# Performance work log

Measured on AMD Instinct MI355X. Metric: run time of the kernel, lower is better.

The kernel has to match this reference:

```python
import jax, jax.numpy as jnp
import numpy as np
import math

B, S, D, H, N = 4, 2048, 1024, 8, 128  # batch, seq_len, d_model, n_heads, num_osc
ITERS = 10
DT = 0.1
PI = math.pi


def setup_inputs() -> dict:
    key = jax.random.key(0)
    ks = jax.random.split(key, 5)
    return {
        "x": jax.random.normal(ks[0], (B, S, D), jnp.float32),
        "mask": jnp.ones((B, S), jnp.int32),
        "W_phase": jax.random.normal(ks[1], (D, H * N), jnp.float32) / math.sqrt(D),
        "b_phase": jnp.zeros((H * N,), jnp.float32),
        "natural_freq": jax.random.normal(ks[2], (H, N), jnp.float32) * 0.1,
        "coupling": jnp.ones((H, 1, 1), jnp.float32),  # coupling_strength = 1.0
        "W_out": jax.random.normal(ks[3], (H * N, D), jnp.float32) / math.sqrt(H * N),
        "b_out": jnp.zeros((D,), jnp.float32),
    }


def reference(x, mask, W_phase, b_phase, natural_freq, coupling, W_out, b_out):
    # phases: [B, H, S, N]
    ph = (x @ W_phase + b_phase).reshape(B, S, H, N).transpose(0, 2, 1, 3)
    ph = jnp.tanh(ph) * PI
    m = mask.astype(ph.dtype)[:, None, :, None]  # [B,1,S,1] mask over j
    K = coupling.reshape(1, H, 1, 1)
    w = natural_freq.reshape(1, H, 1, N)

    def step(ph, _):
        s = jnp.sin(ph)
        c = jnp.cos(ph)
        # mean_j m_j * sin(theta_i - theta_j) = sin(th_i)*mean(m*cos) - cos(th_i)*mean(m*sin)
        ms = (m * s).mean(axis=2, keepdims=True)  # [B,H,1,N]
        mc = (m * c).mean(axis=2, keepdims=True)
        dtheta = w + K * (s * mc - c * ms)
        ph2 = jnp.mod(ph + DT * dtheta + PI, 2 * PI) - PI
        return ph2, None

    ph, _ = jax.lax.scan(step, ph, None, length=ITERS)
    # from_phase; dropout is identity in eval mode
    y = ph.transpose(0, 2, 1, 3).reshape(B, S, H * N) @ W_out + b_out
    return y
```

## Files before the change

kernel.cpp:

```cpp
#include <hip/hip_runtime.h>
#include <math.h>

#define S_ 2048
#define D_ 1024
#define HN_ 1024
#define B_ 4
#define M_ 8192
#define K1_ 3072
#define K3_ 1024
#define ITERS_ 10
#define DT_ 0.1f
#define PI_ 3.14159265358979323846f
#define TWOPI_ 6.28318530717958647692f
#define INV2PI_ 0.15915494309189533577f
#define SCALE_ 4096.0f
#define INVSC2_ (1.0f / 16777216.0f)

typedef __attribute__((ext_vector_type(8))) _Float16 f16x8;
typedef __attribute__((ext_vector_type(4))) float f32x4;

__device__ ushort g_xs [(size_t)M_ * K1_];
__device__ ushort g_WpT[(size_t)HN_ * K1_];
__device__ float  g_ph [(size_t)B_ * HN_ * S_];
__device__ ushort g_phh[(size_t)B_ * HN_ * S_];
__device__ ushort g_phT[(size_t)M_ * HN_];
__device__ ushort g_WoT[(size_t)D_ * HN_];

__device__ __forceinline__ ushort f2h(float f) {
    union { _Float16 h; ushort u; } v; v.h = (_Float16)f; return v.u;
}
__device__ __forceinline__ void split2s(float x, ushort& A, ushort& Bc) {
    const float xs = x * SCALE_;
    union { _Float16 h; ushort u; } va, vb;
    va.h = (_Float16)xs;
    const float r = xs - (float)va.h;
    vb.h = (_Float16)r;
    A = va.u; Bc = vb.u;
}
__device__ __forceinline__ void gload16(const void* g, void* l) {
    __builtin_amdgcn_global_load_lds(
        (const __attribute__((address_space(1))) void*)g,
        (__attribute__((address_space(3))) void*)l, 16, 0, 0);
}
__device__ __forceinline__ int pack2(ushort a, ushort b) {
    return (int)(unsigned)a | ((int)(unsigned)b << 16);
}

__global__ __launch_bounds__(256) void split_x(const float* __restrict__ X) {
    const int idx = blockIdx.x * 256 + threadIdx.x;
    const float4 v = ((const float4*)X)[idx];
    const int m  = idx >> 8;
    const int k4 = (idx & 255) * 4;
    ushort a[4], b[4];
    split2s(v.x, a[0], b[0]);
    split2s(v.y, a[1], b[1]);
    split2s(v.z, a[2], b[2]);
    split2s(v.w, a[3], b[3]);
    ushort* row = g_xs + (size_t)m * K1_ + k4;
    int2 oa; oa.x = pack2(a[0], a[1]); oa.y = pack2(a[2], a[3]);
    int2 ob; ob.x = pack2(b[0], b[1]); ob.y = pack2(b[2], b[3]);
    *(int2*)(row)        = oa;
    *(int2*)(row + 1024) = oa;
    *(int2*)(row + 2048) = ob;
}

__global__ __launch_bounds__(256) void splitT_Wp(const float* __restrict__ Wp) {
    __shared__ float t[64][68];
    const int k0 = blockIdx.x * 64;
    const int n0 = blockIdx.y * 64;
    const int r = threadIdx.x >> 2;
    const int c = (threadIdx.x & 3) * 16;
    const float* src = Wp + (size_t)(k0 + r) * HN_ + n0 + c;
    #pragma unroll
    for (int q = 0; q < 4; ++q)
        *(float4*)&t[r][c + 4 * q] = ((const float4*)src)[q];
    __syncthreads();
    ushort ha[16], hb[16];
    #pragma unroll
    for (int j = 0; j < 16; ++j)
        split2s(t[c + j][r], ha[j], hb[j]);
    int4 a0, a1, b0, b1;
    a0.x = pack2(ha[0], ha[1]);   a0.y = pack2(ha[2], ha[3]);
    a0.z = pack2(ha[4], ha[5]);   a0.w = pack2(ha[6], ha[7]);
    a1.x = pack2(ha[8], ha[9]);   a1.y = pack2(ha[10], ha[11]);
    a1.z = pack2(ha[12], ha[13]); a1.w = pack2(ha[14], ha[15]);
    b0.x = pack2(hb[0], hb[1]);   b0.y = pack2(hb[2], hb[3]);
    b0.z = pack2(hb[4], hb[5]);   b0.w = pack2(hb[6], hb[7]);
    b1.x = pack2(hb[8], hb[9]);   b1.y = pack2(hb[10], hb[11]);
    b1.z = pack2(hb[12], hb[13]); b1.w = pack2(hb[14], hb[15]);
    ushort* dst = g_WpT + (size_t)(n0 + r) * K1_ + k0 + c;
    *(int4*)(dst)            = a0; *(int4*)(dst + 8)        = a1;
    *(int4*)(dst + 1024)     = b0; *(int4*)(dst + 1032)     = b1;
    *(int4*)(dst + 2048)     = a0; *(int4*)(dst + 2056)     = a1;
}

__global__ __launch_bounds__(256) void castT_Wo(const float* __restrict__ Wo) {
    __shared__ float t[64][68];
    const int k0 = blockIdx.x * 64;
    const int n0 = blockIdx.y * 64;
    const int r = threadIdx.x >> 2;
    const int c = (threadIdx.x & 3) * 16;
    const float* src = Wo + (size_t)(k0 + r) * D_ + n0 + c;
    #pragma unroll
    for (int q = 0; q < 4; ++q)
        *(float4*)&t[r][c + 4 * q] = ((const float4*)src)[q];
    __syncthreads();
    ushort h[16];
    #pragma unroll
    for (int j = 0; j < 16; ++j) h[j] = f2h(t[c + j][r]);
    ushort* dst = g_WoT + (size_t)(n0 + r) * HN_ + k0 + c;
    int4 o0, o1;
    o0.x = pack2(h[0], h[1]);   o0.y = pack2(h[2], h[3]);
    o0.z = pack2(h[4], h[5]);   o0.w = pack2(h[6], h[7]);
    o1.x = pack2(h[8], h[9]);   o1.y = pack2(h[10], h[11]);
    o1.z = pack2(h[12], h[13]); o1.w = pack2(h[14], h[15]);
    *(int4*)dst = o0;
    *(int4*)(dst + 8) = o1;
}

template<int KDIM>
__device__ __forceinline__ void gemm_mainloop(const ushort* __restrict__ A,
                                              const ushort* __restrict__ Bm,
                                              ushort* lds,
                                              int m0, int n0, int wid, int l,
                                              int wm, int wn,
                                              f32x4 (&acc)[4][2]) {
    constexpr int NT = KDIM / 64;
    const int r8   = l >> 3;
    const int swzo = ((l & 7) * 16) ^ (r8 << 4);
    const char* gA = (const char*)(A + (size_t)m0 * KDIM);
    const char* gB = (const char*)(Bm + (size_t)n0 * KDIM);

    const int l15 = l & 15;
    const int xk  = (l15 & 7) << 4;
    const int sl0 = (((l >> 4) * 16)) ^ xk;
    const int sl1 = (64 + ((l >> 4) * 16)) ^ xk;
    const char* pA = (const char*)lds + (wm * 64 + l15) * 128;
    const char* pB = (const char*)lds + 16384 + (wn * 32 + l15) * 128;

    #define STAGE(T, BUF) do {                                                    \
        const size_t gb_ = (size_t)(T) * 128 + swzo;                              \
        char* lb_ = (char*)lds + (BUF) * 32768 + wid * 2048;                      \
        gload16(gA + (size_t)(wid * 16 + r8)     * (KDIM * 2) + gb_, lb_);        \
        gload16(gA + (size_t)(wid * 16 + 8 + r8) * (KDIM * 2) + gb_, lb_ + 1024); \
        gload16(gB + (size_t)(wid * 16 + r8)     * (KDIM * 2) + gb_, lb_ + 16384);\
        gload16(gB + (size_t)(wid * 16 + 8 + r8) * (KDIM * 2) + gb_, lb_ + 16384 + 1024); \
    } while (0)

    STAGE(0, 0);

    #pragma unroll 2
    for (int t = 0; t < NT; ++t) {
        __builtin_amdgcn_sched_barrier(0);
        __builtin_amdgcn_s_barrier();
        __builtin_amdgcn_sched_barrier(0);
        if (t + 1 < NT) {
            STAGE(t + 1, (t + 1) & 1);
            asm volatile("s_waitcnt vmcnt(4)" ::: "memory");
        } else {
            asm volatile("s_waitcnt vmcnt(0)" ::: "memory");
        }
        __builtin_amdgcn_sched_barrier(0);
        __builtin_amdgcn_s_barrier();
        __builtin_amdgcn_sched_barrier(0);

        const int bo = (t & 1) << 15;
        f16x8 Aa[4][2], Bb[2][2];
        #pragma unroll
        for (int i = 0; i < 4; ++i) {
            Aa[i][0] = *(const f16x8*)(pA + bo + i * 2048 + sl0);
            Aa[i][1] = *(const f16x8*)(pA + bo + i * 2048 + sl1);
        }
        #pragma unroll
        for (int j = 0; j < 2; ++j) {
            Bb[j][0] = *(const f16x8*)(pB + bo + j * 2048 + sl0);
            Bb[j][1] = *(const f16x8*)(pB + bo + j * 2048 + sl1);
        }
        __builtin_amdgcn_s_setprio(1);
        #pragma unroll
        for (int ks = 0; ks < 2; ++ks)
            #pragma unroll
            for (int i = 0; i < 4; ++i)
                #pragma unroll
                for (int j = 0; j < 2; ++j)
                    acc[i][j] = __builtin_amdgcn_mfma_f32_16x16x32_f16(
                        Aa[i][ks], Bb[j][ks], acc[i][j], 0, 0, 0);
        __builtin_amdgcn_s_setprio(0);
    }
    #undef STAGE
}

__device__ __forceinline__ void tile_map(int bid, int& m0, int& n0) {
    const int xcd = bid & 7;
    const int idx = bid >> 3;
    m0 = (xcd * 8 + (idx >> 3)) * 128;
    n0 = (idx & 7) * 128;
}

__global__ __launch_bounds__(512, 4) void gemm1(const float* __restrict__ bias) {
    __shared__ ushort lds[2 * 16384];
    const int tid = threadIdx.x;
    const int wid = tid >> 6, l = tid & 63;
    int m0, n0;
    tile_map(blockIdx.x, m0, n0);
    const int wm = wid >> 2, wn = wid & 3;

    f32x4 acc[4][2];
    #pragma unroll
    for (int i = 0; i < 4; ++i)
        #pragma unroll
        for (int j = 0; j < 2; ++j) acc[i][j] = (f32x4){0.f, 0.f, 0.f, 0.f};

    gemm_mainloop<K1_>(g_xs, g_WpT, lds, m0, n0, wid, l, wm, wn, acc);

    const int r4 = (l >> 4) * 4;
    const int cn = l & 15;
    #pragma unroll
    for (int i = 0; i < 4; ++i) {
        const int mg = m0 + wm * 64 + i * 16 + r4;
        const int bidx = mg >> 11;
        const int sg = mg & 2047;
        #pragma unroll
        for (int jj = 0; jj < 2; ++jj) {
            const int ng = n0 + wn * 32 + jj * 16 + cn;
            const float bb = bias[ng];
            float4 o;
            o.x = PI_ * tanhf(fmaf(acc[i][jj][0], INVSC2_, bb));
            o.y = PI_ * tanhf(fmaf(acc[i][jj][1], INVSC2_, bb));
            o.z = PI_ * tanhf(fmaf(acc[i][jj][2], INVSC2_, bb));
            o.w = PI_ * tanhf(fmaf(acc[i][jj][3], INVSC2_, bb));
            *(float4*)(g_ph + ((size_t)bidx * HN_ + ng) * S_ + sg) = o;
        }
    }
}

__global__ __launch_bounds__(512, 4) void gemm3(const float* __restrict__ bias,
                                                float* __restrict__ Y) {
    __shared__ ushort lds[2 * 16384];
    const int tid = threadIdx.x;
    const int wid = tid >> 6, l = tid & 63;
    int m0, n0;
    tile_map(blockIdx.x, m0, n0);
    const int wm = wid >> 2, wn = wid & 3;

    f32x4 acc[4][2];
    #pragma unroll
    for (int i = 0; i < 4; ++i)
        #pragma unroll
        for (int j = 0; j < 2; ++j) acc[i][j] = (f32x4){0.f, 0.f, 0.f, 0.f};

    gemm_mainloop<K3_>(g_phT, g_WoT, lds, m0, n0, wid, l, wm, wn, acc);

    const int r4 = (l >> 4) * 4;
    const int cn = l & 15;
    #pragma unroll
    for (int i = 0; i < 4; ++i) {
        const int mg = m0 + wm * 64 + i * 16 + r4;
        #pragma unroll
        for (int jj = 0; jj < 2; ++jj) {
            const int ng = n0 + wn * 32 + jj * 16 + cn;
            const float bb = bias[ng];
            #pragma unroll
            for (int r = 0; r < 4; ++r)
                Y[(size_t)(mg + r) * D_ + ng] = acc[i][jj][r] + bb;
        }
    }
}

__global__ __launch_bounds__(256) void kuramoto(const int* __restrict__ mask,
                                                const float* __restrict__ natf,
                                                const float* __restrict__ coup) {
    const int wave = blockIdx.x * 4 + (threadIdx.x >> 6);
    const int lane = threadIdx.x & 63;
    const int b = wave >> 10;
    const int hn = wave & 1023;
    const int h = hn >> 7;

    const float wf = natf[hn];
    const float K = coup[h];

    const float* base = g_ph + ((size_t)b * HN_ + hn) * S_;

    float ph[32];
    #pragma unroll
    for (int i = 0; i < 8; ++i) {
        float4 v = *(const float4*)(base + i * 256 + lane * 4);
        ph[4 * i + 0] = v.x; ph[4 * i + 1] = v.y;
        ph[4 * i + 2] = v.z; ph[4 * i + 3] = v.w;
    }

    const int* mb = mask + b * S_;
    unsigned mbits = 0;
    #pragma unroll
    for (int i = 0; i < 8; ++i) {
        int4 mv = *(const int4*)(mb + i * 256 + lane * 4);
        mbits |= (mv.x != 0 ? 1u : 0u) << (4 * i + 0);
        mbits |= (mv.y != 0 ? 1u : 0u) << (4 * i + 1);
        mbits |= (mv.z != 0 ? 1u : 0u) << (4 * i + 2);
        mbits |= (mv.w != 0 ? 1u : 0u) << (4 * i + 3);
    }

    for (int it = 0; it < ITERS_; ++it) {
        float s[32], c[32];
        float ls = 0.f, lc = 0.f;
        #pragma unroll
        for (int i = 0; i < 32; ++i) {
            s[i] = __sinf(ph[i]);
            c[i] = __cosf(ph[i]);
            const float mf = (float)((mbits >> i) & 1u);
            ls = fmaf(mf, s[i], ls);
            lc = fmaf(mf, c[i], lc);
        }
        #pragma unroll
        for (int off = 32; off; off >>= 1) {
            ls += __shfl_xor(ls, off);
            lc += __shfl_xor(lc, off);
        }
        const float ms = ls * (1.f / 2048.f);
        const float mc = lc * (1.f / 2048.f);
        #pragma unroll
        for (int i = 0; i < 32; ++i) {
            const float dth = fmaf(K, fmaf(s[i], mc, -c[i] * ms), wf);
            float t = fmaf(DT_, dth, ph[i]) + PI_;
            t -= TWOPI_ * floorf(t * INV2PI_);
            ph[i] = t - PI_;
        }
    }

    ushort* ob = g_phh + ((size_t)b * HN_ + hn) * S_;
    #pragma unroll
    for (int i = 0; i < 8; ++i) {
        ushort4 o;
        o.x = f2h(ph[4 * i + 0]); o.y = f2h(ph[4 * i + 1]);
        o.z = f2h(ph[4 * i + 2]); o.w = f2h(ph[4 * i + 3]);
        *(ushort4*)(ob + i * 256 + lane * 4) = o;
    }
}

__global__ __launch_bounds__(256) void transpose_ph() {
    __shared__ ushort t[64][72];
    const int b = blockIdx.z;
    const int h0 = blockIdx.y * 64;
    const int s0 = blockIdx.x * 64;
    const int r = threadIdx.x >> 2;
    const int c = (threadIdx.x & 3) * 16;
    const ushort* src = g_phh + ((size_t)b * HN_ + h0 + r) * S_ + s0 + c;
    *(int4*)&t[r][c] = *(const int4*)src;
    *(int4*)&t[r][c + 8] = *(const int4*)(src + 8);
    __syncthreads();
    ushort o[16];
    #pragma unroll
    for (int j = 0; j < 16; ++j) o[j] = t[c + j][r];
    ushort* dst = g_phT + ((size_t)(b * S_ + s0 + r)) * HN_ + h0 + c;
    int4 o0, o1;
    o0.x = pack2(o[0], o[1]);   o0.y = pack2(o[2], o[3]);
    o0.z = pack2(o[4], o[5]);   o0.w = pack2(o[6], o[7]);
    o1.x = pack2(o[8], o[9]);   o1.y = pack2(o[10], o[11]);
    o1.z = pack2(o[12], o[13]); o1.w = pack2(o[14], o[15]);
    *(int4*)dst = o0;
    *(int4*)(dst + 8) = o1;
}

extern "C" void kernel_launch(void* const* d_in, const int* in_sizes, int n_in,
                              void* d_out, int out_size, void* d_ws, size_t ws_size,
                              hipStream_t stream) {
    const float* x    = (const float*)d_in[0];
    const int*   mask = (const int*)d_in[1];
    const float* Wp   = (const float*)d_in[2];
    const float* bp   = (const float*)d_in[3];
    const float* natf = (const float*)d_in[4];
    const float* coup = (const float*)d_in[5];
    const float* Wo   = (const float*)d_in[6];
    const float* bo   = (const float*)d_in[7];
    float* y = (float*)d_out;

    split_x  <<<dim3(8192),         256, 0, stream>>>(x);
    splitT_Wp<<<dim3(16, 16),       256, 0, stream>>>(Wp);
    castT_Wo <<<dim3(16, 16),       256, 0, stream>>>(Wo);
    gemm1    <<<dim3(512),          512, 0, stream>>>(bp);
    kuramoto <<<dim3(1024),         256, 0, stream>>>(mask, natf, coup);
    transpose_ph<<<dim3(32, 16, 4), 256, 0, stream>>>();
    gemm3    <<<dim3(512),          512, 0, stream>>>(bo, y);
}
```

Before: 166.2 us.

## Pre-fragment weights into MFMA register layout and load B directly from global

Weights are repacked into a fragment-major layout so each lane can load its MFMA B operand straight from global memory into registers, with no LDS staging. The split-fp16 A operand shrinks from three copies to two (hi and lo), and the loop visits the hi part twice, once against the weight hi and once against the weight lo. LDS use per block is halved and the main loop is unrolled by two with explicit double buffering. B loads now go through the vector memory path, which may add latency and repeat global traffic across blocks that share the same weights.

```diff
diff --git a/kernel.cpp b/kernel.cpp
--- a/kernel.cpp
+++ b/kernel.cpp
@@ -6,8 +6,6 @@
 #define HN_ 1024
 #define B_ 4
 #define M_ 8192
-#define K1_ 3072
-#define K3_ 1024
 #define ITERS_ 10
 #define DT_ 0.1f
 #define PI_ 3.14159265358979323846f
@@ -19,12 +17,12 @@
 typedef __attribute__((ext_vector_type(8))) _Float16 f16x8;
 typedef __attribute__((ext_vector_type(4))) float f32x4;
 
-__device__ ushort g_xs [(size_t)M_ * K1_];
-__device__ ushort g_WpT[(size_t)HN_ * K1_];
-__device__ float  g_ph [(size_t)B_ * HN_ * S_];
-__device__ ushort g_phh[(size_t)B_ * HN_ * S_];
-__device__ ushort g_phT[(size_t)M_ * HN_];
-__device__ ushort g_WoT[(size_t)D_ * HN_];
+__device__ __align__(16) ushort g_xs [(size_t)M_ * 2048];
+__device__ __align__(16) ushort g_WpB[(size_t)64 * 64 * 512];
+__device__ __align__(16) ushort g_WoB[(size_t)64 * 32 * 512];
+__device__ __align__(16) float  g_ph [(size_t)B_ * HN_ * S_];
+__device__ __align__(16) ushort g_phh[(size_t)B_ * HN_ * S_];
+__device__ __align__(16) ushort g_phT[(size_t)M_ * HN_];
 
 __device__ __forceinline__ ushort f2h(float f) {
     union { _Float16 h; ushort u; } v; v.h = (_Float16)f; return v.u;
@@ -56,138 +54,158 @@
     split2s(v.y, a[1], b[1]);
     split2s(v.z, a[2], b[2]);
     split2s(v.w, a[3], b[3]);
-    ushort* row = g_xs + (size_t)m * K1_ + k4;
+    ushort* row = g_xs + (size_t)m * 2048 + k4;
     int2 oa; oa.x = pack2(a[0], a[1]); oa.y = pack2(a[2], a[3]);
     int2 ob; ob.x = pack2(b[0], b[1]); ob.y = pack2(b[2], b[3]);
     *(int2*)(row)        = oa;
-    *(int2*)(row + 1024) = oa;
-    *(int2*)(row + 2048) = ob;
-}
-
-__global__ __launch_bounds__(256) void splitT_Wp(const float* __restrict__ Wp) {
-    __shared__ float t[64][68];
-    const int k0 = blockIdx.x * 64;
-    const int n0 = blockIdx.y * 64;
-    const int r = threadIdx.x >> 2;
-    const int c = (threadIdx.x & 3) * 16;
-    const float* src = Wp + (size_t)(k0 + r) * HN_ + n0 + c;
-    #pragma unroll
-    for (int q = 0; q < 4; ++q)
-        *(float4*)&t[r][c + 4 * q] = ((const float4*)src)[q];
+    *(int2*)(row + 1024) = ob;
+}
+
+__global__ __launch_bounds__(128) void prep_WpB(const float* __restrict__ Wp) {
+    __shared__ float t[64][17];
+    const int kc = blockIdx.x, n16 = blockIdx.y;
+    const int k0 = kc * 64, nb = n16 * 16;
+    {
+        const int r = threadIdx.x >> 1, hf = (threadIdx.x & 1) * 8;
+        const float* src = Wp + (size_t)(k0 + r) * HN_ + nb + hf;
+        *(float4*)&t[r][hf]     = *(const float4*)src;
+        *(float4*)&t[r][hf + 4] = *(const float4*)(src + 4);
+    }
     __syncthreads();
-    ushort ha[16], hb[16];
-    #pragma unroll
-    for (int j = 0; j < 16; ++j)
-        split2s(t[c + j][r], ha[j], hb[j]);
-    int4 a0, a1, b0, b1;
-    a0.x = pack2(ha[0], ha[1]);   a0.y = pack2(ha[2], ha[3]);
-    a0.z = pack2(ha[4], ha[5]);   a0.w = pack2(ha[6], ha[7]);
-    a1.x = pack2(ha[8], ha[9]);   a1.y = pack2(ha[10], ha[11]);
-    a1.z = pack2(ha[12], ha[13]); a1.w = pack2(ha[14], ha[15]);
-    b0.x = pack2(hb[0], hb[1]);   b0.y = pack2(hb[2], hb[3]);
-    b0.z = pack2(hb[4], hb[5]);   b0.w = pack2(hb[6], hb[7]);
-    b1.x = pack2(hb[8], hb[9]);   b1.y = pack2(hb[10], hb[11]);
-    b1.z = pack2(hb[12], hb[13]); b1.w = pack2(hb[14], hb[15]);
-    ushort* dst = g_WpT + (size_t)(n0 + r) * K1_ + k0 + c;
-    *(int4*)(dst)            = a0; *(int4*)(dst + 8)        = a1;
-    *(int4*)(dst + 1024)     = b0; *(int4*)(dst + 1032)     = b1;
-    *(int4*)(dst + 2048)     = a0; *(int4*)(dst + 2056)     = a1;
-}
-
-__global__ __launch_bounds__(256) void castT_Wo(const float* __restrict__ Wo) {
-    __shared__ float t[64][68];
-    const int k0 = blockIdx.x * 64;
-    const int n0 = blockIdx.y * 64;
-    const int r = threadIdx.x >> 2;
-    const int c = (threadIdx.x & 3) * 16;
-    const float* src = Wo + (size_t)(k0 + r) * D_ + n0 + c;
-    #pragma unroll
-    for (int q = 0; q < 4; ++q)
-        *(float4*)&t[r][c + 4 * q] = ((const float4*)src)[q];
+    const int h = threadIdx.x >> 6, l = threadIdx.x & 63;
+    const int n = l & 15, ks8 = (l >> 4) * 8;
+    ushort ua[8], ub[8];
+    #pragma unroll
+    for (int j = 0; j < 8; ++j)
+        split2s(t[h * 32 + ks8 + j][n], ua[j], ub[j]);
+    const int kt32a = kc * 2 + h;
+    ushort* da = g_WpB + ((size_t)(n16 * 64 + kt32a) * 64 + l) * 8;
+    ushort* db = g_WpB + ((size_t)(n16 * 64 + 32 + kt32a) * 64 + l) * 8;
+    int4 oa, ob;
+    oa.x = pack2(ua[0], ua[1]); oa.y = pack2(ua[2], ua[3]);
+    oa.z = pack2(ua[4], ua[5]); oa.w = pack2(ua[6], ua[7]);
+    ob.x = pack2(ub[0], ub[1]); ob.y = pack2(ub[2], ub[3]);
+    ob.z = pack2(ub[4], ub[5]); ob.w = pack2(ub[6], ub[7]);
+    *(int4*)da = oa;
+    *(int4*)db = ob;
+}
+
+__global__ __launch_bounds__(128) void prep_WoB(const float* __restrict__ Wo) {
+    __shared__ float t[64][17];
+    const int kc = blockIdx.x, n16 = blockIdx.y;
+    const int k0 = kc * 64, nb = n16 * 16;
+    {
+        const int r = threadIdx.x >> 1, hf = (threadIdx.x & 1) * 8;
+        const float* src = Wo + (size_t)(k0 + r) * D_ + nb + hf;
+        *(float4*)&t[r][hf]     = *(const float4*)src;
+        *(float4*)&t[r][hf + 4] = *(const float4*)(src + 4);
+    }
     __syncthreads();
-    ushort h[16];
-    #pragma unroll
-    for (int j = 0; j < 16; ++j) h[j] = f2h(t[c + j][r]);
-    ushort* dst = g_WoT + (size_t)(n0 + r) * HN_ + k0 + c;
-    int4 o0, o1;
-    o0.x = pack2(h[0], h[1]);   o0.y = pack2(h[2], h[3]);
-    o0.z = pack2(h[4], h[5]);   o0.w = pack2(h[6], h[7]);
-    o1.x = pack2(h[8], h[9]);   o1.y = pack2(h[10], h[11]);
-    o1.z = pack2(h[12], h[13]); o1.w = pack2(h[14], h[15]);
-    *(int4*)dst = o0;
-    *(int4*)(dst + 8) = o1;
-}
-
-template<int KDIM>
+    const int h = threadIdx.x >> 6, l = threadIdx.x & 63;
+    const int n = l & 15, ks8 = (l >> 4) * 8;
+    ushort u[8];
+    #pragma unroll
+    for (int j = 0; j < 8; ++j) u[j] = f2h(t[h * 32 + ks8 + j][n]);
+    const int kt32 = kc * 2 + h;
+    ushort* d = g_WoB + ((size_t)(n16 * 32 + kt32) * 64 + l) * 8;
+    int4 o;
+    o.x = pack2(u[0], u[1]); o.y = pack2(u[2], u[3]);
+    o.z = pack2(u[4], u[5]); o.w = pack2(u[6], u[7]);
+    *(int4*)d = o;
+}
+
+template<int NT, int SPLIT>
 __device__ __forceinline__ void gemm_mainloop(const ushort* __restrict__ A,
-                                              const ushort* __restrict__ Bm,
+                                              const ushort* __restrict__ Bf,
                                               ushort* lds,
                                               int m0, int n0, int wid, int l,
                                               int wm, int wn,
                                               f32x4 (&acc)[4][2]) {
-    constexpr int NT = KDIM / 64;
+    constexpr int K2   = SPLIT ? 2048 : 1024;
+    constexpr int NK32 = SPLIT ? 64 : 32;
     const int r8   = l >> 3;
     const int swzo = ((l & 7) * 16) ^ (r8 << 4);
-    const char* gA = (const char*)(A + (size_t)m0 * KDIM);
-    const char* gB = (const char*)(Bm + (size_t)n0 * KDIM);
-
+    const char* gA = (const char*)(A + (size_t)m0 * K2);
     const int l15 = l & 15;
     const int xk  = (l15 & 7) << 4;
     const int sl0 = (((l >> 4) * 16)) ^ xk;
     const int sl1 = (64 + ((l >> 4) * 16)) ^ xk;
     const char* pA = (const char*)lds + (wm * 64 + l15) * 128;
-    const char* pB = (const char*)lds + 16384 + (wn * 32 + l15) * 128;
-
-    #define STAGE(T, BUF) do {                                                    \
-        const size_t gb_ = (size_t)(T) * 128 + swzo;                              \
-        char* lb_ = (char*)lds + (BUF) * 32768 + wid * 2048;                      \
-        gload16(gA + (size_t)(wid * 16 + r8)     * (KDIM * 2) + gb_, lb_);        \
-        gload16(gA + (size_t)(wid * 16 + 8 + r8) * (KDIM * 2) + gb_, lb_ + 1024); \
-        gload16(gB + (size_t)(wid * 16 + r8)     * (KDIM * 2) + gb_, lb_ + 16384);\
-        gload16(gB + (size_t)(wid * 16 + 8 + r8) * (KDIM * 2) + gb_, lb_ + 16384 + 1024); \
+    const ushort* pB0 = Bf + (size_t)(((n0 >> 4) + wn * 2 + 0) * NK32) * 512 + l * 8;
+    const ushort* pB1 = Bf + (size_t)(((n0 >> 4) + wn * 2 + 1) * NK32) * 512 + l * 8;
+
+    #define AOFFB(T) ((size_t)((SPLIT && (T) >= 16) ? (T) - 16 : (T)) * 128)
+    #define KT32(T)  ((SPLIT && (T) >= 32) ? 2 * (T) - 64 : 2 * (T))
+
+    #define STAGE_A(T, BUF) do {                                                  \
+        const size_t gb_ = AOFFB(T) + swzo;                                       \
+        char* lb_ = (char*)lds + (BUF) * 16384 + wid * 2048;                      \
+        gload16(gA + (size_t)(wid * 16 + r8)     * (K2 * 2) + gb_, lb_);          \
+        gload16(gA + (size_t)(wid * 16 + 8 + r8) * (K2 * 2) + gb_, lb_ + 1024);   \
     } while (0)
 
-    STAGE(0, 0);
-
-    #pragma unroll 2
-    for (int t = 0; t < NT; ++t) {
-        __builtin_amdgcn_sched_barrier(0);
-        __builtin_amdgcn_s_barrier();
-        __builtin_amdgcn_sched_barrier(0);
-        if (t + 1 < NT) {
-            STAGE(t + 1, (t + 1) & 1);
-            asm volatile("s_waitcnt vmcnt(4)" ::: "memory");
+    #define LOADB(T, BR) do {                                                     \
+        const int kb_ = KT32(T);                                                  \
+        BR[0][0] = *(const f16x8*)(pB0 + (size_t)kb_ * 512);                      \
+        BR[0][1] = *(const f16x8*)(pB0 + (size_t)(kb_ + 1) * 512);                \
+        BR[1][0] = *(const f16x8*)(pB1 + (size_t)kb_ * 512);                      \
+        BR[1][1] = *(const f16x8*)(pB1 + (size_t)(kb_ + 1) * 512);                \
+    } while (0)
+
+    #define SB __builtin_amdgcn_sched_barrier(0)
+    #define LDA(BO) do {                                                          \
+        _Pragma("unroll")                                                         \
+        for (int i_ = 0; i_ < 4; ++i_) {                                          \
+            Aa[i_][0] = *(const f16x8*)(pA + (BO) + i_ * 2048 + sl0);             \
+            Aa[i_][1] = *(const f16x8*)(pA + (BO) + i_ * 2048 + sl1);             \
+        }                                                                         \
+    } while (0)
+    #define MFMA_BLK(BR) do {                                                     \
+        __builtin_amdgcn_s_setprio(1);                                            \
+        _Pragma("unroll")                                                         \
+        for (int ks_ = 0; ks_ < 2; ++ks_)                                         \
+            _Pragma("unroll")                                                     \
+            for (int i_ = 0; i_ < 4; ++i_)                                        \
+                _Pragma("unroll")                                                 \
+                for (int j_ = 0; j_ < 2; ++j_)                                    \
+                    acc[i_][j_] = __builtin_amdgcn_mfma_f32_16x16x32_f16(         \
+                        Aa[i_][ks_], BR[j_][ks_], acc[i_][j_], 0, 0, 0);          \
+        __builtin_amdgcn_s_setprio(0);                                            \
+    } while (0)
+
+    f16x8 Ba[2][2], Bb[2][2];
+    f16x8 Aa[4][2];
+
+    LOADB(0, Ba);
+    STAGE_A(0, 0);
+
+    for (int t = 0; t < NT; t += 2) {
+        SB; __builtin_amdgcn_s_barrier(); SB;
+        LOADB(t + 1, Bb);
+        STAGE_A(t + 1, 1);
+        asm volatile("s_waitcnt vmcnt(6)" ::: "memory");
+        SB; __builtin_amdgcn_s_barrier(); SB;
+        LDA(0);
+        MFMA_BLK(Ba);
+        SB; __builtin_amdgcn_s_barrier(); SB;
+        if (t + 2 < NT) {
+            LOADB(t + 2, Ba);
+            STAGE_A(t + 2, 0);
+            asm volatile("s_waitcnt vmcnt(6)" ::: "memory");
         } else {
             asm volatile("s_waitcnt vmcnt(0)" ::: "memory");
         }
-        __builtin_amdgcn_sched_barrier(0);
-        __builtin_amdgcn_s_barrier();
-        __builtin_amdgcn_sched_barrier(0);
-
-        const int bo = (t & 1) << 15;
-        f16x8 Aa[4][2], Bb[2][2];
-        #pragma unroll
-        for (int i = 0; i < 4; ++i) {
-            Aa[i][0] = *(const f16x8*)(pA + bo + i * 2048 + sl0);
-            Aa[i][1] = *(const f16x8*)(pA + bo + i * 2048 + sl1);
-        }
-        #pragma unroll
-        for (int j = 0; j < 2; ++j) {
-            Bb[j][0] = *(const f16x8*)(pB + bo + j * 2048 + sl0);
-            Bb[j][1] = *(const f16x8*)(pB + bo + j * 2048 + sl1);
-        }
-        __builtin_amdgcn_s_setprio(1);
-        #pragma unroll
-        for (int ks = 0; ks < 2; ++ks)
-            #pragma unroll
-            for (int i = 0; i < 4; ++i)
-                #pragma unroll
-                for (int j = 0; j < 2; ++j)
-                    acc[i][j] = __builtin_amdgcn_mfma_f32_16x16x32_f16(
-                        Aa[i][ks], Bb[j][ks], acc[i][j], 0, 0, 0);
-        __builtin_amdgcn_s_setprio(0);
-    }
-    #undef STAGE
+        SB; __builtin_amdgcn_s_barrier(); SB;
+        LDA(16384);
+        MFMA_BLK(Bb);
+    }
+    #undef STAGE_A
+    #undef LOADB
+    #undef LDA
+    #undef MFMA_BLK
+    #undef SB
+    #undef AOFFB
+    #undef KT32
 }
 
 __device__ __forceinline__ void tile_map(int bid, int& m0, int& n0) {
@@ -198,7 +216,7 @@
 }
 
 __global__ __launch_bounds__(512, 4) void gemm1(const float* __restrict__ bias) {
-    __shared__ ushort lds[2 * 16384];
+    __shared__ ushort lds[2 * 8192];
     const int tid = threadIdx.x;
     const int wid = tid >> 6, l = tid & 63;
     int m0, n0;
@@ -211,7 +229,7 @@
         #pragma unroll
         for (int j = 0; j < 2; ++j) acc[i][j] = (f32x4){0.f, 0.f, 0.f, 0.f};
 
-    gemm_mainloop<K1_>(g_xs, g_WpT, lds, m0, n0, wid, l, wm, wn, acc);
+    gemm_mainloop<48, 1>(g_xs, g_WpB, lds, m0, n0, wid, l, wm, wn, acc);
 
     const int r4 = (l >> 4) * 4;
     const int cn = l & 15;
@@ -236,7 +254,7 @@
 
 __global__ __launch_bounds__(512, 4) void gemm3(const float* __restrict__ bias,
                                                 float* __restrict__ Y) {
-    __shared__ ushort lds[2 * 16384];
+    __shared__ ushort lds[2 * 8192];
     const int tid = threadIdx.x;
     const int wid = tid >> 6, l = tid & 63;
     int m0, n0;
@@ -249,7 +267,7 @@
         #pragma unroll
         for (int j = 0; j < 2; ++j) acc[i][j] = (f32x4){0.f, 0.f, 0.f, 0.f};
 
-    gemm_mainloop<K3_>(g_phT, g_WoT, lds, m0, n0, wid, l, wm, wn, acc);
+    gemm_mainloop<16, 0>(g_phT, g_WoB, lds, m0, n0, wid, l, wm, wn, acc);
 
     const int r4 = (l >> 4) * 4;
     const int cn = l & 15;
@@ -375,8 +393,8 @@
     float* y = (float*)d_out;
 
     split_x  <<<dim3(8192),         256, 0, stream>>>(x);
-    splitT_Wp<<<dim3(16, 16),       256, 0, stream>>>(Wp);
-    castT_Wo <<<dim3(16, 16),       256, 0, stream>>>(Wo);
+    prep_WpB <<<dim3(16, 64),       128, 0, stream>>>(Wp);
+    prep_WoB <<<dim3(16, 64),       128, 0, stream>>>(Wo);
     gemm1    <<<dim3(512),          512, 0, stream>>>(bp);
     kuramoto <<<dim3(1024),         256, 0, stream>>>(mask, natf, coup);
     transpose_ph<<<dim3(32, 16, 4), 256, 0, stream>>>();
```

Result: no change. 167.4 us (+0.7%).

## Store split operands once and remap K offsets; merge prep kernels

Applied to the files above, without the earlier changes.

The split-fp16 GEMM1 operands used to be stored with a duplicated third K-segment (K=3072), so hi/lo products could be formed by plain contiguous K. They are now stored with K=2048 (hi, lo), and the mainloop remaps each K-tile to the right segment of A and B through offset macros. That cuts the prep write traffic and GEMM1 operand footprint by about a third while keeping 48 K-tiles. The three prep kernels are also fused into one launch, saving launch overhead. The risks are more complex address arithmetic and a less regular access pattern across K-tiles.

```diff
diff --git a/kernel.cpp b/kernel.cpp
--- a/kernel.cpp
+++ b/kernel.cpp
@@ -6,8 +6,6 @@
 #define HN_ 1024
 #define B_ 4
 #define M_ 8192
-#define K1_ 3072
-#define K3_ 1024
 #define ITERS_ 10
 #define DT_ 0.1f
 #define PI_ 3.14159265358979323846f
@@ -19,12 +17,12 @@
 typedef __attribute__((ext_vector_type(8))) _Float16 f16x8;
 typedef __attribute__((ext_vector_type(4))) float f32x4;
 
-__device__ ushort g_xs [(size_t)M_ * K1_];
-__device__ ushort g_WpT[(size_t)HN_ * K1_];
-__device__ float  g_ph [(size_t)B_ * HN_ * S_];
-__device__ ushort g_phh[(size_t)B_ * HN_ * S_];
-__device__ ushort g_phT[(size_t)M_ * HN_];
-__device__ ushort g_WoT[(size_t)D_ * HN_];
+__device__ __align__(16) ushort g_xs [(size_t)M_ * 2048];
+__device__ __align__(16) ushort g_WpT[(size_t)HN_ * 2048];
+__device__ __align__(16) ushort g_WoT[(size_t)D_ * 1024];
+__device__ __align__(16) float  g_ph [(size_t)B_ * HN_ * S_];
+__device__ __align__(16) ushort g_phh[(size_t)B_ * HN_ * S_];
+__device__ __align__(16) ushort g_phT[(size_t)M_ * HN_];
 
 __device__ __forceinline__ ushort f2h(float f) {
     union { _Float16 h; ushort u; } v; v.h = (_Float16)f; return v.u;
@@ -46,91 +44,89 @@
     return (int)(unsigned)a | ((int)(unsigned)b << 16);
 }
 
-__global__ __launch_bounds__(256) void split_x(const float* __restrict__ X) {
-    const int idx = blockIdx.x * 256 + threadIdx.x;
-    const float4 v = ((const float4*)X)[idx];
-    const int m  = idx >> 8;
-    const int k4 = (idx & 255) * 4;
-    ushort a[4], b[4];
-    split2s(v.x, a[0], b[0]);
-    split2s(v.y, a[1], b[1]);
-    split2s(v.z, a[2], b[2]);
-    split2s(v.w, a[3], b[3]);
-    ushort* row = g_xs + (size_t)m * K1_ + k4;
-    int2 oa; oa.x = pack2(a[0], a[1]); oa.y = pack2(a[2], a[3]);
-    int2 ob; ob.x = pack2(b[0], b[1]); ob.y = pack2(b[2], b[3]);
-    *(int2*)(row)        = oa;
-    *(int2*)(row + 1024) = oa;
-    *(int2*)(row + 2048) = ob;
-}
-
-__global__ __launch_bounds__(256) void splitT_Wp(const float* __restrict__ Wp) {
+__global__ __launch_bounds__(256) void prep(const float* __restrict__ X,
+                                            const float* __restrict__ Wp,
+                                            const float* __restrict__ Wo) {
     __shared__ float t[64][68];
-    const int k0 = blockIdx.x * 64;
-    const int n0 = blockIdx.y * 64;
-    const int r = threadIdx.x >> 2;
-    const int c = (threadIdx.x & 3) * 16;
-    const float* src = Wp + (size_t)(k0 + r) * HN_ + n0 + c;
+    const int bid = blockIdx.x;
+    const int tid = threadIdx.x;
+    if (bid < 2048) {
+        #pragma unroll
+        for (int p = 0; p < 4; ++p) {
+            const int idx = bid * 1024 + p * 256 + tid;
+            const float4 v = ((const float4*)X)[idx];
+            const int m  = idx >> 8;
+            const int k4 = (idx & 255) * 4;
+            ushort a[4], b[4];
+            split2s(v.x, a[0], b[0]);
+            split2s(v.y, a[1], b[1]);
+            split2s(v.z, a[2], b[2]);
+            split2s(v.w, a[3], b[3]);
+            ushort* row = g_xs + (size_t)m * 2048 + k4;
+            int2 oa; oa.x = pack2(a[0], a[1]); oa.y = pack2(a[2], a[3]);
+            int2 ob; ob.x = pack2(b[0], b[1]); ob.y = pack2(b[2], b[3]);
+            *(int2*)(row)        = oa;
+            *(int2*)(row + 1024) = ob;
+        }
+        return;
+    }
+    const int wb   = bid - 2048;
+    const bool isWp = (wb < 256);
+    const int g  = isWp ? wb : wb - 256;
+    const int k0 = (g >> 4) * 64;
+    const int n0 = (g & 15) * 64;
+    const int r = tid >> 2;
+    const int c = (tid & 3) * 16;
+    const float* src = (isWp ? Wp : Wo) + (size_t)(k0 + r) * 1024 + n0 + c;
     #pragma unroll
     for (int q = 0; q < 4; ++q)
         *(float4*)&t[r][c + 4 * q] = ((const float4*)src)[q];
     __syncthreads();
-    ushort ha[16], hb[16];
-    #pragma unroll
-    for (int j = 0; j < 16; ++j)
-        split2s(t[c + j][r], ha[j], hb[j]);
-    int4 a0, a1, b0, b1;
-    a0.x = pack2(ha[0], ha[1]);   a0.y = pack2(ha[2], ha[3]);
-    a0.z = pack2(ha[4], ha[5]);   a0.w = pack2(ha[6], ha[7]);
-    a1.x = pack2(ha[8], ha[9]);   a1.y = pack2(ha[10], ha[11]);
-    a1.z = pack2(ha[12], ha[13]); a1.w = pack2(ha[14], ha[15]);
-    b0.x = pack2(hb[0], hb[1]);   b0.y = pack2(hb[2], hb[3]);
-    b0.z = pack2(hb[4], hb[5]);   b0.w = pack2(hb[6], hb[7]);
-    b1.x = pack2(hb[8], hb[9]);   b1.y = pack2(hb[10], hb[11]);
-    b1.z = pack2(hb[12], hb[13]); b1.w = pack2(hb[14], hb[15]);
-    ushort* dst = g_WpT + (size_t)(n0 + r) * K1_ + k0 + c;
-    *(int4*)(dst)            = a0; *(int4*)(dst + 8)        = a1;
-    *(int4*)(dst + 1024)     = b0; *(int4*)(dst + 1032)     = b1;
-    *(int4*)(dst + 2048)     = a0; *(int4*)(dst + 2056)     = a1;
-}
-
-__global__ __launch_bounds__(256) void castT_Wo(const float* __restrict__ Wo) {
-    __shared__ float t[64][68];
-    const int k0 = blockIdx.x * 64;
-    const int n0 = blockIdx.y * 64;
-    const int r = threadIdx.x >> 2;
-    const int c = (threadIdx.x & 3) * 16;
-    const float* src = Wo + (size_t)(k0 + r) * D_ + n0 + c;
-    #pragma unroll
-    for (int q = 0; q < 4; ++q)
-        *(float4*)&t[r][c + 4 * q] = ((const float4*)src)[q];
-    __syncthreads();
-    ushort h[16];
-    #pragma unroll
-    for (int j = 0; j < 16; ++j) h[j] = f2h(t[c + j][r]);
-    ushort* dst = g_WoT + (size_t)(n0 + r) * HN_ + k0 + c;
-    int4 o0, o1;
-    o0.x = pack2(h[0], h[1]);   o0.y = pack2(h[2], h[3]);
-    o0.z = pack2(h[4], h[5]);   o0.w = pack2(h[6], h[7]);
-    o1.x = pack2(h[8], h[9]);   o1.y = pack2(h[10], h[11]);
-    o1.z = pack2(h[12], h[13]); o1.w = pack2(h[14], h[15]);
-    *(int4*)dst = o0;
-    *(int4*)(dst + 8) = o1;
-}
-
-template<int KDIM>
+    if (isWp) {
+        ushort ha[16], hb[16];
+        #pragma unroll
+        for (int j = 0; j < 16; ++j)
+            split2s(t[c + j][r], ha[j], hb[j]);
+        int4 a0, a1, b0, b1;
+        a0.x = pack2(ha[0], ha[1]);   a0.y = pack2(ha[2], ha[3]);
+        a0.z = pack2(ha[4], ha[5]);   a0.w = pack2(ha[6], ha[7]);
+        a1.x = pack2(ha[8], ha[9]);   a1.y = pack2(ha[10], ha[11]);
+        a1.z = pack2(ha[12], ha[13]); a1.w = pack2(ha[14], ha[15]);
+        b0.x = pack2(hb[0], hb[1]);   b0.y = pack2(hb[2], hb[3]);
+        b0.z = pack2(hb[4], hb[5]);   b0.w = pack2(hb[6], hb[7]);
+        b1.x = pack2(hb[8], hb[9]);   b1.y = pack2(hb[10], hb[11]);
+        b1.z = pack2(hb[12], hb[13]); b1.w = pack2(hb[14], hb[15]);
+        ushort* dst = g_WpT + (size_t)(n0 + r) * 2048 + k0 + c;
+        *(int4*)(dst)        = a0; *(int4*)(dst + 8)    = a1;
+        *(int4*)(dst + 1024) = b0; *(int4*)(dst + 1032) = b1;
+    } else {
+        ushort h[16];
+        #pragma unroll
+        for (int j = 0; j < 16; ++j) h[j] = f2h(t[c + j][r]);
+        ushort* dst = g_WoT + (size_t)(n0 + r) * 1024 + k0 + c;
+        int4 o0, o1;
+        o0.x = pack2(h[0], h[1]);   o0.y = pack2(h[2], h[3]);
+        o0.z = pack2(h[4], h[5]);   o0.w = pack2(h[6], h[7]);
+        o1.x = pack2(h[8], h[9]);   o1.y = pack2(h[10], h[11]);
+        o1.z = pack2(h[12], h[13]); o1.w = pack2(h[14], h[15]);
+        *(int4*)dst = o0;
+        *(int4*)(dst + 8) = o1;
+    }
+}
+
+template<int NT, int SPLIT>
 __device__ __forceinline__ void gemm_mainloop(const ushort* __restrict__ A,
                                               const ushort* __restrict__ Bm,
                                               ushort* lds,
                                               int m0, int n0, int wid, int l,
-                                              int wm, int wn,
                                               f32x4 (&acc)[4][2]) {
-    constexpr int NT = KDIM / 64;
+    constexpr int KROW = SPLIT ? 2048 : 1024;
     const int r8   = l >> 3;
     const int swzo = ((l & 7) * 16) ^ (r8 << 4);
-    const char* gA = (const char*)(A + (size_t)m0 * KDIM);
-    const char* gB = (const char*)(Bm + (size_t)n0 * KDIM);
-
+    const char* gA = (const char*)(A + (size_t)m0 * KROW);
+    const char* gB = (const char*)(Bm + (size_t)n0 * KROW);
+
+    const int wm = wid >> 2, wn = wid & 3;
     const int l15 = l & 15;
     const int xk  = (l15 & 7) << 4;
     const int sl0 = (((l >> 4) * 16)) ^ xk;
@@ -138,13 +134,20 @@
     const char* pA = (const char*)lds + (wm * 64 + l15) * 128;
     const char* pB = (const char*)lds + 16384 + (wn * 32 + l15) * 128;
 
+    #define AOFF(T) ((size_t)(SPLIT ? ((T) < 32 ? ((T) & 15) * 128 : 2048 + ((T) - 32) * 128) \
+                                    : (T) * 128))
+    #define BOFF(T) ((size_t)(SPLIT ? ((T) < 16 ? (T) * 128                                   \
+                                     : ((T) < 32 ? 2048 + ((T) - 16) * 128                    \
+                                                 : ((T) - 32) * 128))                         \
+                                    : (T) * 128))
+
     #define STAGE(T, BUF) do {                                                    \
-        const size_t gb_ = (size_t)(T) * 128 + swzo;                              \
+        const size_t ao_ = AOFF(T) + swzo, bo_ = BOFF(T) + swzo;                  \
         char* lb_ = (char*)lds + (BUF) * 32768 + wid * 2048;                      \
-        gload16(gA + (size_t)(wid * 16 + r8)     * (KDIM * 2) + gb_, lb_);        \
-        gload16(gA + (size_t)(wid * 16 + 8 + r8) * (KDIM * 2) + gb_, lb_ + 1024); \
-        gload16(gB + (size_t)(wid * 16 + r8)     * (KDIM * 2) + gb_, lb_ + 16384);\
-        gload16(gB + (size_t)(wid * 16 + 8 + r8) * (KDIM * 2) + gb_, lb_ + 16384 + 1024); \
+        gload16(gA + (size_t)(wid * 16 + r8)     * (KROW * 2) + ao_, lb_);        \
+        gload16(gA + (size_t)(wid * 16 + 8 + r8) * (KROW * 2) + ao_, lb_ + 1024); \
+        gload16(gB + (size_t)(wid * 16 + r8)     * (KROW * 2) + bo_, lb_ + 16384);\
+        gload16(gB + (size_t)(wid * 16 + 8 + r8) * (KROW * 2) + bo_, lb_ + 16384 + 1024); \
     } while (0)
 
     STAGE(0, 0);
@@ -188,6 +191,8 @@
         __builtin_amdgcn_s_setprio(0);
     }
     #undef STAGE
+    #undef AOFF
+    #undef BOFF
 }
 
 __device__ __forceinline__ void tile_map(int bid, int& m0, int& n0) {
@@ -211,7 +216,7 @@
         #pragma unroll
         for (int j = 0; j < 2; ++j) acc[i][j] = (f32x4){0.f, 0.f, 0.f, 0.f};
 
-    gemm_mainloop<K1_>(g_xs, g_WpT, lds, m0, n0, wid, l, wm, wn, acc);
+    gemm_mainloop<48, 1>(g_xs, g_WpT, lds, m0, n0, wid, l, acc);
 
     const int r4 = (l >> 4) * 4;
     const int cn = l & 15;
@@ -249,7 +254,7 @@
         #pragma unroll
         for (int j = 0; j < 2; ++j) acc[i][j] = (f32x4){0.f, 0.f, 0.f, 0.f};
 
-    gemm_mainloop<K3_>(g_phT, g_WoT, lds, m0, n0, wid, l, wm, wn, acc);
+    gemm_mainloop<16, 0>(g_phT, g_WoT, lds, m0, n0, wid, l, acc);
 
     const int r4 = (l >> 4) * 4;
     const int cn = l & 15;
@@ -374,11 +379,9 @@
     const float* bo   = (const float*)d_in[7];
     float* y = (float*)d_out;
 
-    split_x  <<<dim3(8192),         256, 0, stream>>>(x);
-    splitT_Wp<<<dim3(16, 16),       256, 0, stream>>>(Wp);
-    castT_Wo <<<dim3(16, 16),       256, 0, stream>>>(Wo);
-    gemm1    <<<dim3(512),          512, 0, stream>>>(bp);
-    kuramoto <<<dim3(1024),         256, 0, stream>>>(mask, natf, coup);
+    prep        <<<dim3(2560),      256, 0, stream>>>(x, Wp, Wo);
+    gemm1       <<<dim3(512),       512, 0, stream>>>(bp);
+    kuramoto    <<<dim3(1024),      256, 0, stream>>>(mask, natf, coup);
     transpose_ph<<<dim3(32, 16, 4), 256, 0, stream>>>();
-    gemm3    <<<dim3(512),          512, 0, stream>>>(bo, y);
-}
+    gemm3       <<<dim3(512),       512, 0, stream>>>(bo, y);
+}
```

Measured after the change: 159.3 us. 1.04x faster.
